# Optimization experiments

Hardware: AMD Instinct MI355X
Metric: run time of the kernel (lower is better)

## Reference

```python
import jax, jax.numpy as jnp
import numpy as np

BSZ, T, D_IN, P, H, D_OUT = 8, 4096, 512, 256, 256, 512


def setup_inputs() -> dict:
    key = jax.random.key(0)
    ks = jax.random.split(key, 8)
    x_seq = jax.random.normal(ks[0], (BSZ, T, D_IN), dtype=jnp.float32)
    # stable diagonal transition: |a| < 1 so the 4096-step recurrence does not blow up
    a = jax.random.uniform(ks[1], (H,), minval=-0.99, maxval=0.99, dtype=jnp.float32)
    B = jax.random.normal(ks[2], (P, H), dtype=jnp.float32) * 0.05
    C = jax.random.normal(ks[3], (H, P), dtype=jnp.float32) * 0.05
    Wi = jax.random.normal(ks[4], (P, D_IN), dtype=jnp.float32) * 0.05
    bi = jax.random.normal(ks[5], (P,), dtype=jnp.float32) * 0.05
    Wo = jax.random.normal(ks[6], (D_OUT, P), dtype=jnp.float32) * 0.05
    bo = jax.random.normal(ks[7], (D_OUT,), dtype=jnp.float32) * 0.05
    return {"x_seq": x_seq, "a": a, "B": B, "C": C, "Wi": Wi, "bi": bi, "Wo": Wo, "bo": bo}


def reference(x_seq, a, B, C, Wi, bi, Wo, bo):
    # proj_in + relu (eqx.nn.Linear: y = W @ x + b), vmapped over batch and time
    x_proj = jax.nn.relu(jnp.einsum("btd,pd->btp", x_seq, Wi) + bi)  # [Bsz,T,P]
    # precompute driving input u_t = B^T x_t for every step
    u = jnp.einsum("btp,ph->bth", x_proj, B)  # [Bsz,T,H]
    u_t = jnp.swapaxes(u, 0, 1)  # [T,Bsz,H] (scan over time)

    def step(h, u_step):  # h: [Bsz,H]
        h = a * h + u_step
        return h, h

    h0 = jnp.zeros((x_seq.shape[0], a.shape[0]), dtype=x_seq.dtype)
    _, hs = jax.lax.scan(step, h0, u_t)  # hs: [T,Bsz,H]
    # y_t = C^T h_t, then proj_out
    y_seq = jnp.einsum("tbh,hp->btp", hs, C)  # [Bsz,T,P]
    y_out = jnp.einsum("btp,op->bto", y_seq, Wo) + bo  # [Bsz,T,D_out]
    return y_out
```

## Files before the change

### kernel.cpp

```cpp
#include <hip/hip_runtime.h>

#define BSZN 8
#define TT 4096
#define DIN 512
#define PP 256
#define HHH 256
#define DOUT 512
#define LCH 64
#define NCH (TT / LCH)
#define NBLK (BSZN * NCH)
#define XTS 520
#define XPS 264

typedef __attribute__((ext_vector_type(8))) short bf16x8;
typedef __attribute__((ext_vector_type(4))) float f32x4;

static __device__ __forceinline__ unsigned short f2bf(float x) {
  union { float f; unsigned u; } t{x};
  unsigned r = t.u + 0x7fffu + ((t.u >> 16) & 1u);
  return (unsigned short)(r >> 16);
}


__global__ __launch_bounds__(256) void prep_k(
    const float* __restrict__ Wi, const float* __restrict__ Wo,
    const float* __restrict__ Cm, const float* __restrict__ Bm,
    unsigned short* __restrict__ Wi_t, unsigned short* __restrict__ B_t,
    unsigned short* __restrict__ C_t, unsigned short* __restrict__ Wo_t) {
  const int b = blockIdx.x, tid = threadIdx.x;
  if (b < 128) {
    const int idx = b * 1024 + tid * 4;
    const int row = idx >> 9, d = idx & 511;
    const float4 v = *(const float4*)(Wi + idx);
    uint2 w;
    w.x = (unsigned)f2bf(v.x) | ((unsigned)f2bf(v.y) << 16);
    w.y = (unsigned)f2bf(v.z) | ((unsigned)f2bf(v.w) << 16);
    const int tile = d >> 5, kc = (d >> 3) & 3, s = (kc + (row >> 1)) & 3;
    *(uint2*)(Wi_t + tile * 8192 + row * 32 + s * 8 + (d & 7)) = w;
  } else if (b < 192) {
    const int f = (b - 128) * 256 + tid;
    const int p = f >> 6, h = (f & 63) * 4;
    const float4 v = *(const float4*)(Bm + (size_t)p * HHH + h);
    const float vv[4] = {v.x, v.y, v.z, v.w};
    const int tile = p >> 5, kc = (p >> 3) & 3;
#pragma unroll
    for (int j = 0; j < 4; ++j) {
      const int row = h + j, s = (kc + (row >> 1)) & 3;
      B_t[tile * 8192 + row * 32 + s * 8 + (p & 7)] = f2bf(vv[j]);
    }
  } else if (b < 256) {
    const int f = (b - 192) * 256 + tid;
    const int h = f >> 6, p = (f & 63) * 4;
    const float4 v = *(const float4*)(Cm + (size_t)h * PP + p);
    const float vv[4] = {v.x, v.y, v.z, v.w};
    const int tile = h >> 5, kc = (h >> 3) & 3;
#pragma unroll
    for (int j = 0; j < 4; ++j) {
      const int row = p + j, s = (kc + (row >> 1)) & 3;
      C_t[tile * 8192 + row * 32 + s * 8 + (h & 7)] = f2bf(vv[j]);
    }
  } else {
    const int idx = (b - 256) * 1024 + tid * 4;
    const int o = idx >> 8, p = idx & 255;
    const float4 v = *(const float4*)(Wo + idx);
    uint2 w;
    w.x = (unsigned)f2bf(v.x) | ((unsigned)f2bf(v.y) << 16);
    w.y = (unsigned)f2bf(v.z) | ((unsigned)f2bf(v.w) << 16);
    const int tile = p >> 5, kc = (p >> 3) & 3, s = (kc + (o >> 1)) & 3;
    *(uint2*)(Wo_t + tile * 16384 + o * 32 + s * 8 + (p & 7)) = w;
  }
}

__global__ __launch_bounds__(256, 2) void s4_scan(
    const float* __restrict__ x, const float* __restrict__ a,
    const unsigned short* __restrict__ Wi_t, const float* __restrict__ bi,
    const unsigned short* __restrict__ B_t, float* __restrict__ hs0_g,
    float* __restrict__ carry_g) {
  __shared__ alignas(16) char smem[66560];
  unsigned short* xs = (unsigned short*)smem;
  unsigned short* xp = (unsigned short*)smem;

  const int tid = threadIdx.x, wave = tid >> 6, lane = tid & 63;
  const int l15 = lane & 15, q = lane >> 4;
  const int bc = blockIdx.x;
  const size_t row0 = (size_t)bc * LCH;
  const int wc = wave * 64;

  int wrot[4];
#pragma unroll
  for (int ni = 0; ni < 4; ++ni) {
    const int r = wc + ni * 16 + l15;
    wrot[ni] = r * 64 + (((q + (r >> 1)) & 3) << 4);
  }
  int xsb[4];
#pragma unroll
  for (int mi = 0; mi < 4; ++mi) xsb[mi] = (mi * 16 + l15) * (XTS * 2) + q * 16;
  int xpb[4];
#pragma unroll
  for (int mi = 0; mi < 4; ++mi) xpb[mi] = (mi * 16 + l15) * XPS + q * 8;

#pragma unroll
  for (int rr = 0; rr < 2; ++rr) {
    float4 xv[16];
#pragma unroll
    for (int i = 0; i < 16; ++i) {
      const int f = rr * 4096 + i * 256 + tid;
      xv[i] = *(const float4*)(x + (row0 + (f >> 7)) * DIN + (f & 127) * 4);
    }
#pragma unroll
    for (int i = 0; i < 16; ++i) {
      const int f = rr * 4096 + i * 256 + tid;
      uint2 w;
      w.x = (unsigned)f2bf(xv[i].x) | ((unsigned)f2bf(xv[i].y) << 16);
      w.y = (unsigned)f2bf(xv[i].z) | ((unsigned)f2bf(xv[i].w) << 16);
      *(uint2*)(xs + (f >> 7) * XTS + (f & 127) * 4) = w;
    }
  }
  __syncthreads();

  f32x4 acc[4][4];
#pragma unroll
  for (int i = 0; i < 4; ++i)
#pragma unroll
    for (int j = 0; j < 4; ++j) acc[i][j] = f32x4{0.f, 0.f, 0.f, 0.f};
  {
    const char* WiB = (const char*)Wi_t;
    for (int t = 0; t < 8; ++t) {
      bf16x8 af[4][2], bfv[4][2];
#pragma unroll
      for (int mi = 0; mi < 4; ++mi) {
        af[mi][0] = *(const bf16x8*)((const char*)xs + xsb[mi] + t * 128);
        af[mi][1] = *(const bf16x8*)((const char*)xs + xsb[mi] + t * 128 + 64);
      }
#pragma unroll
      for (int ni = 0; ni < 4; ++ni) {
        bfv[ni][0] = *(const bf16x8*)(WiB + t * 32768 + wrot[ni]);
        bfv[ni][1] = *(const bf16x8*)(WiB + t * 32768 + 16384 + wrot[ni]);
      }
#pragma unroll
      for (int kk = 0; kk < 2; ++kk)
#pragma unroll
        for (int mi = 0; mi < 4; ++mi)
#pragma unroll
          for (int ni = 0; ni < 4; ++ni)
            acc[mi][ni] = __builtin_amdgcn_mfma_f32_16x16x32_bf16(
                af[mi][kk], bfv[ni][kk], acc[mi][ni], 0, 0, 0);
    }
  }
  __syncthreads();

#pragma unroll
  for (int ni = 0; ni < 4; ++ni) {
    const int col = wc + ni * 16 + l15;
    const float bb = bi[col];
#pragma unroll
    for (int mi = 0; mi < 4; ++mi)
#pragma unroll
      for (int reg = 0; reg < 4; ++reg) {
        const int row = mi * 16 + q * 4 + reg;
        xp[row * XPS + col] = f2bf(fmaxf(acc[mi][ni][reg] + bb, 0.f));
      }
  }
  __syncthreads();

#pragma unroll
  for (int i = 0; i < 4; ++i)
#pragma unroll
    for (int j = 0; j < 4; ++j) acc[i][j] = f32x4{0.f, 0.f, 0.f, 0.f};
  {
    const char* BB = (const char*)B_t;
    for (int t = 0; t < 4; ++t) {
      bf16x8 af[4][2], bfv[4][2];
#pragma unroll
      for (int mi = 0; mi < 4; ++mi) {
        af[mi][0] = *(const bf16x8*)(xp + xpb[mi] + t * 64);
        af[mi][1] = *(const bf16x8*)(xp + xpb[mi] + t * 64 + 32);
      }
#pragma unroll
      for (int ni = 0; ni < 4; ++ni) {
        bfv[ni][0] = *(const bf16x8*)(BB + t * 32768 + wrot[ni]);
        bfv[ni][1] = *(const bf16x8*)(BB + t * 32768 + 16384 + wrot[ni]);
      }
#pragma unroll
      for (int kk = 0; kk < 2; ++kk)
#pragma unroll
        for (int mi = 0; mi < 4; ++mi)
#pragma unroll
          for (int ni = 0; ni < 4; ++ni)
            acc[mi][ni] = __builtin_amdgcn_mfma_f32_16x16x32_bf16(
                af[mi][kk], bfv[ni][kk], acc[mi][ni], 0, 0, 0);
    }
  }

  float aC[4], Wz[4];
#pragma unroll
  for (int ni = 0; ni < 4; ++ni) aC[ni] = a[wc + ni * 16 + l15];
#pragma unroll
  for (int ni = 0; ni < 4; ++ni) {
    const float A = aC[ni];
    const float A2 = A * A, A4 = A2 * A2, A8 = A4 * A4, A16 = A8 * A8;
    const float A4q = ((q & 1) ? A4 : 1.f) * ((q & 2) ? A8 : 1.f);
    float W = 0.f;
#pragma unroll
    for (int mi = 0; mi < 4; ++mi) {
      f32x4 v = acc[mi][ni];
      v.y = fmaf(A, v.x, v.y);
      v.z = fmaf(A, v.y, v.z);
      v.w = fmaf(A, v.z, v.w);
      const float E = v.w;
      const float E0 = __shfl(E, l15, 64);
      const float E1 = __shfl(E, l15 + 16, 64);
      const float E2 = __shfl(E, l15 + 32, 64);
      const float E3 = __shfl(E, l15 + 48, 64);
      const float s1 = E0, s2 = fmaf(A4, s1, E1), s3 = fmaf(A4, s2, E2);
      const float s4 = fmaf(A4, s3, E3);
      const float Sq = (q == 0) ? 0.f : (q == 1) ? s1 : (q == 2) ? s2 : s3;
      const float sin_ = fmaf(A4q, W, Sq);
      v.x = fmaf(A, sin_, v.x);
      v.y = fmaf(A2, sin_, v.y);
      v.z = fmaf(A2 * A, sin_, v.z);
      v.w = fmaf(A4, sin_, v.w);
      acc[mi][ni] = v;
      W = fmaf(A16, W, s4);
    }
    Wz[ni] = W;
  }
  if (q == 0) {
#pragma unroll
    for (int ni = 0; ni < 4; ++ni)
      carry_g[(size_t)bc * HHH + wc + ni * 16 + l15] = Wz[ni];
  }
#pragma unroll
  for (int ni = 0; ni < 4; ++ni)
#pragma unroll
    for (int mi = 0; mi < 4; ++mi) {
      const size_t idx =
          ((((size_t)bc * 4 + wave) * 16 + ni * 4 + mi) * 64 + lane) * 4;
      *(f32x4*)(hs0_g + idx) = acc[mi][ni];
    }
}

__global__ __launch_bounds__(256) void s4_prefix(
    const float* __restrict__ a, const float* __restrict__ carry_g,
    float* __restrict__ P_g) {
  const int b = blockIdx.x, t = threadIdx.x;
  float A = a[t];
#pragma unroll
  for (int j = 0; j < 6; ++j) A *= A;
  const float* cg = carry_g + (size_t)b * NCH * HHH + t;
  float* pg = P_g + (size_t)b * NCH * HHH + t;
  float cv[NCH];
#pragma unroll
  for (int c = 0; c < NCH; ++c) cv[c] = cg[(size_t)c * HHH];
  float P = 0.f;
#pragma unroll
  for (int c = 0; c < NCH; ++c) {
    pg[(size_t)c * HHH] = P;
    P = fmaf(A, P, cv[c]);
  }
}

__global__ __launch_bounds__(256, 2) void s4_out(
    const float* __restrict__ a, const float* __restrict__ hs0_g,
    const float* __restrict__ P_g, const unsigned short* __restrict__ C_t,
    const unsigned short* __restrict__ Wo_t, const float* __restrict__ bo,
    float* __restrict__ out) {
  __shared__ alignas(16) char smem[33792];
  unsigned short* hsL = (unsigned short*)smem;

  const int tid = threadIdx.x, wave = tid >> 6, lane = tid & 63;
  const int l15 = lane & 15, q = lane >> 4;
  const int bc = blockIdx.x;
  const size_t row0 = (size_t)bc * LCH;
  const int wc = wave * 64;

  int wrot[4];
#pragma unroll
  for (int ni = 0; ni < 4; ++ni) {
    const int r = wc + ni * 16 + l15;
    wrot[ni] = r * 64 + (((q + (r >> 1)) & 3) << 4);
  }
  int crot[2][4];
#pragma unroll
  for (int g = 0; g < 2; ++g)
#pragma unroll
    for (int ni = 0; ni < 4; ++ni) {
      const int r = wave * 128 + g * 64 + ni * 16 + l15;
      crot[g][ni] = r * 64 + (((q + (r >> 1)) & 3) << 4);
    }
  int xpb[4];
#pragma unroll
  for (int mi = 0; mi < 4; ++mi) xpb[mi] = (mi * 16 + l15) * XPS + q * 8;

  f32x4 acc[4][4];
#pragma unroll
  for (int ni = 0; ni < 4; ++ni)
#pragma unroll
    for (int mi = 0; mi < 4; ++mi) {
      const size_t idx =
          ((((size_t)bc * 4 + wave) * 16 + ni * 4 + mi) * 64 + lane) * 4;
      acc[mi][ni] = *(const f32x4*)(hs0_g + idx);
    }
#pragma unroll
  for (int ni = 0; ni < 4; ++ni) {
    const int col = wc + ni * 16 + l15;
    const float A = a[col];
    const float P = P_g[(size_t)bc * HHH + col];
    const float A2 = A * A, A4 = A2 * A2, A8 = A4 * A4, A16 = A8 * A8;
    const float A4q = ((q & 1) ? A4 : 1.f) * ((q & 2) ? A8 : 1.f);
    float fm = A4q * A * P;
#pragma unroll
    for (int mi = 0; mi < 4; ++mi) {
      f32x4 v = acc[mi][ni];
      v.x += fm;
      v.y = fmaf(A, fm, v.y);
      v.z = fmaf(A2, fm, v.z);
      v.w = fmaf(A2 * A, fm, v.w);
      acc[mi][ni] = v;
      fm *= A16;
    }
  }
#pragma unroll
  for (int ni = 0; ni < 4; ++ni) {
    const int col = wc + ni * 16 + l15;
#pragma unroll
    for (int mi = 0; mi < 4; ++mi)
#pragma unroll
      for (int reg = 0; reg < 4; ++reg)
        hsL[(mi * 16 + q * 4 + reg) * XPS + col] = f2bf(acc[mi][ni][reg]);
  }
  __syncthreads();

#pragma unroll
  for (int i = 0; i < 4; ++i)
#pragma unroll
    for (int j = 0; j < 4; ++j) acc[i][j] = f32x4{0.f, 0.f, 0.f, 0.f};
  {
    const char* CB = (const char*)C_t;
    for (int t = 0; t < 4; ++t) {
      bf16x8 af[4][2], bfv[4][2];
#pragma unroll
      for (int mi = 0; mi < 4; ++mi) {
        af[mi][0] = *(const bf16x8*)(hsL + xpb[mi] + t * 64);
        af[mi][1] = *(const bf16x8*)(hsL + xpb[mi] + t * 64 + 32);
      }
#pragma unroll
      for (int ni = 0; ni < 4; ++ni) {
        bfv[ni][0] = *(const bf16x8*)(CB + t * 32768 + wrot[ni]);
        bfv[ni][1] = *(const bf16x8*)(CB + t * 32768 + 16384 + wrot[ni]);
      }
#pragma unroll
      for (int kk = 0; kk < 2; ++kk)
#pragma unroll
        for (int mi = 0; mi < 4; ++mi)
#pragma unroll
          for (int ni = 0; ni < 4; ++ni)
            acc[mi][ni] = __builtin_amdgcn_mfma_f32_16x16x32_bf16(
                af[mi][kk], bfv[ni][kk], acc[mi][ni], 0, 0, 0);
    }
  }
  __syncthreads();

#pragma unroll
  for (int ni = 0; ni < 4; ++ni) {
    const int col = wc + ni * 16 + l15;
#pragma unroll
    for (int mi = 0; mi < 4; ++mi)
#pragma unroll
      for (int reg = 0; reg < 4; ++reg)
        hsL[(mi * 16 + q * 4 + reg) * XPS + col] = f2bf(acc[mi][ni][reg]);
  }
  __syncthreads();

  f32x4 oacc[2][4][4];
#pragma unroll
  for (int g = 0; g < 2; ++g)
#pragma unroll
    for (int i = 0; i < 4; ++i)
#pragma unroll
      for (int j = 0; j < 4; ++j) oacc[g][i][j] = f32x4{0.f, 0.f, 0.f, 0.f};
  {
    const char* WoB = (const char*)Wo_t;
    for (int t = 0; t < 8; ++t) {
      bf16x8 af[4], bfv[2][4];
#pragma unroll
      for (int mi = 0; mi < 4; ++mi)
        af[mi] = *(const bf16x8*)(hsL + xpb[mi] + t * 32);
#pragma unroll
      for (int g = 0; g < 2; ++g)
#pragma unroll
        for (int ni = 0; ni < 4; ++ni)
          bfv[g][ni] = *(const bf16x8*)(WoB + t * 32768 + crot[g][ni]);
#pragma unroll
      for (int g = 0; g < 2; ++g)
#pragma unroll
        for (int mi = 0; mi < 4; ++mi)
#pragma unroll
          for (int ni = 0; ni < 4; ++ni)
            oacc[g][mi][ni] = __builtin_amdgcn_mfma_f32_16x16x32_bf16(
                af[mi], bfv[g][ni], oacc[g][mi][ni], 0, 0, 0);
    }
  }
#pragma unroll
  for (int g = 0; g < 2; ++g)
#pragma unroll
    for (int ni = 0; ni < 4; ++ni) {
      const int ocol = wave * 128 + g * 64 + ni * 16 + l15;
      const float bb = bo[ocol];
#pragma unroll
      for (int mi = 0; mi < 4; ++mi)
#pragma unroll
        for (int reg = 0; reg < 4; ++reg) {
          const int row = mi * 16 + q * 4 + reg;
          out[(row0 + row) * DOUT + ocol] = oacc[g][mi][ni][reg] + bb;
        }
    }
}

extern "C" void kernel_launch(void* const* d_in, const int* in_sizes, int n_in,
                              void* d_out, int out_size, void* d_ws,
                              size_t ws_size, hipStream_t stream) {
  const float* x  = (const float*)d_in[0];
  const float* a  = (const float*)d_in[1];
  const float* Bm = (const float*)d_in[2];
  const float* Cm = (const float*)d_in[3];
  const float* Wi = (const float*)d_in[4];
  const float* bi = (const float*)d_in[5];
  const float* Wo = (const float*)d_in[6];
  const float* bo = (const float*)d_in[7];
  float* out = (float*)d_out;

  char* ws = (char*)d_ws;
  unsigned short* Wi_t = (unsigned short*)ws; ws += (size_t)PP * DIN * 2;
  unsigned short* B_t  = (unsigned short*)ws; ws += (size_t)HHH * PP * 2;
  unsigned short* C_t  = (unsigned short*)ws; ws += (size_t)HHH * PP * 2;
  unsigned short* Wo_t = (unsigned short*)ws; ws += (size_t)DOUT * PP * 2;
  float* carry_g = (float*)ws; ws += (size_t)NBLK * HHH * 4;
  float* P_g     = (float*)ws; ws += (size_t)NBLK * HHH * 4;
  float* hs0_g   = (float*)ws;

  prep_k<<<384, 256, 0, stream>>>(Wi, Wo, Cm, Bm, Wi_t, B_t, C_t, Wo_t);
  s4_scan<<<NBLK, 256, 0, stream>>>(x, a, Wi_t, bi, B_t, hs0_g, carry_g);
  s4_prefix<<<BSZN, 256, 0, stream>>>(a, carry_g, P_g);
  s4_out<<<NBLK, 256, 0, stream>>>(a, hs0_g, P_g, C_t, Wo_t, bo, out);
}
```

Baseline: 161.4 us.

## Halve scan chunk length, split x staging by K, store intermediate states in bf16

```diff
diff --git a/kernel.cpp b/kernel.cpp
--- a/kernel.cpp
+++ b/kernel.cpp
@@ -6,10 +6,9 @@
 #define PP 256
 #define HHH 256
 #define DOUT 512
-#define LCH 64
+#define LCH 32
 #define NCH (TT / LCH)
 #define NBLK (BSZN * NCH)
-#define XTS 520
 #define XPS 264
 
 typedef __attribute__((ext_vector_type(8))) short bf16x8;
@@ -71,12 +70,12 @@
   }
 }
 
-__global__ __launch_bounds__(256, 2) void s4_scan(
+__global__ __launch_bounds__(256, 4) void s4_scan(
     const float* __restrict__ x, const float* __restrict__ a,
     const unsigned short* __restrict__ Wi_t, const float* __restrict__ bi,
-    const unsigned short* __restrict__ B_t, float* __restrict__ hs0_g,
+    const unsigned short* __restrict__ B_t, unsigned int* __restrict__ hs0_g,
     float* __restrict__ carry_g) {
-  __shared__ alignas(16) char smem[66560];
+  __shared__ alignas(16) char smem[16896];
   unsigned short* xs = (unsigned short*)smem;
   unsigned short* xp = (unsigned short*)smem;
 
@@ -92,69 +91,66 @@
     const int r = wc + ni * 16 + l15;
     wrot[ni] = r * 64 + (((q + (r >> 1)) & 3) << 4);
   }
-  int xsb[4];
-#pragma unroll
-  for (int mi = 0; mi < 4; ++mi) xsb[mi] = (mi * 16 + l15) * (XTS * 2) + q * 16;
-  int xpb[4];
-#pragma unroll
-  for (int mi = 0; mi < 4; ++mi) xpb[mi] = (mi * 16 + l15) * XPS + q * 8;
-
-#pragma unroll
-  for (int rr = 0; rr < 2; ++rr) {
-    float4 xv[16];
-#pragma unroll
-    for (int i = 0; i < 16; ++i) {
-      const int f = rr * 4096 + i * 256 + tid;
-      xv[i] = *(const float4*)(x + (row0 + (f >> 7)) * DIN + (f & 127) * 4);
-    }
-#pragma unroll
-    for (int i = 0; i < 16; ++i) {
-      const int f = rr * 4096 + i * 256 + tid;
-      uint2 w;
-      w.x = (unsigned)f2bf(xv[i].x) | ((unsigned)f2bf(xv[i].y) << 16);
-      w.y = (unsigned)f2bf(xv[i].z) | ((unsigned)f2bf(xv[i].w) << 16);
-      *(uint2*)(xs + (f >> 7) * XTS + (f & 127) * 4) = w;
-    }
-  }
-  __syncthreads();
-
-  f32x4 acc[4][4];
-#pragma unroll
-  for (int i = 0; i < 4; ++i)
+  int xpb[2];
+#pragma unroll
+  for (int mi = 0; mi < 2; ++mi) xpb[mi] = (mi * 16 + l15) * XPS + q * 8;
+
+  f32x4 acc[2][4];
+#pragma unroll
+  for (int i = 0; i < 2; ++i)
 #pragma unroll
     for (int j = 0; j < 4; ++j) acc[i][j] = f32x4{0.f, 0.f, 0.f, 0.f};
-  {
-    const char* WiB = (const char*)Wi_t;
-    for (int t = 0; t < 8; ++t) {
-      bf16x8 af[4][2], bfv[4][2];
-#pragma unroll
-      for (int mi = 0; mi < 4; ++mi) {
-        af[mi][0] = *(const bf16x8*)((const char*)xs + xsb[mi] + t * 128);
-        af[mi][1] = *(const bf16x8*)((const char*)xs + xsb[mi] + t * 128 + 64);
+
+  for (int hh = 0; hh < 2; ++hh) {
+    {
+      float4 xv[8];
+#pragma unroll
+      for (int i = 0; i < 8; ++i) {
+        const int f = i * 256 + tid;
+        xv[i] = *(const float4*)(x + (row0 + (f >> 6)) * DIN + hh * 256 +
+                                 (f & 63) * 4);
+      }
+#pragma unroll
+      for (int i = 0; i < 8; ++i) {
+        const int f = i * 256 + tid;
+        uint2 w;
+        w.x = (unsigned)f2bf(xv[i].x) | ((unsigned)f2bf(xv[i].y) << 16);
+        w.y = (unsigned)f2bf(xv[i].z) | ((unsigned)f2bf(xv[i].w) << 16);
+        *(uint2*)(xs + (f >> 6) * XPS + (f & 63) * 4) = w;
+      }
+    }
+    __syncthreads();
+    const char* WiB = (const char*)Wi_t + hh * 8 * 16384;
+    for (int t = 0; t < 4; ++t) {
+      bf16x8 af[2][2], bfv[4][2];
+#pragma unroll
+      for (int mi = 0; mi < 2; ++mi) {
+        af[mi][0] = *(const bf16x8*)(xs + xpb[mi] + t * 64);
+        af[mi][1] = *(const bf16x8*)(xs + xpb[mi] + t * 64 + 32);
       }
 #pragma unroll
       for (int ni = 0; ni < 4; ++ni) {
-        bfv[ni][0] = *(const bf16x8*)(WiB + t * 32768 + wrot[ni]);
-        bfv[ni][1] = *(const bf16x8*)(WiB + t * 32768 + 16384 + wrot[ni]);
+        bfv[ni][0] = *(const bf16x8*)(WiB + (t * 2) * 16384 + wrot[ni]);
+        bfv[ni][1] = *(const bf16x8*)(WiB + (t * 2 + 1) * 16384 + wrot[ni]);
       }
 #pragma unroll
       for (int kk = 0; kk < 2; ++kk)
 #pragma unroll
-        for (int mi = 0; mi < 4; ++mi)
+        for (int mi = 0; mi < 2; ++mi)
 #pragma unroll
           for (int ni = 0; ni < 4; ++ni)
             acc[mi][ni] = __builtin_amdgcn_mfma_f32_16x16x32_bf16(
                 af[mi][kk], bfv[ni][kk], acc[mi][ni], 0, 0, 0);
     }
-  }
-  __syncthreads();
+    __syncthreads();
+  }
 
 #pragma unroll
   for (int ni = 0; ni < 4; ++ni) {
     const int col = wc + ni * 16 + l15;
     const float bb = bi[col];
 #pragma unroll
-    for (int mi = 0; mi < 4; ++mi)
+    for (int mi = 0; mi < 2; ++mi)
 #pragma unroll
       for (int reg = 0; reg < 4; ++reg) {
         const int row = mi * 16 + q * 4 + reg;
@@ -164,27 +160,27 @@
   __syncthreads();
 
 #pragma unroll
-  for (int i = 0; i < 4; ++i)
+  for (int i = 0; i < 2; ++i)
 #pragma unroll
     for (int j = 0; j < 4; ++j) acc[i][j] = f32x4{0.f, 0.f, 0.f, 0.f};
   {
     const char* BB = (const char*)B_t;
     for (int t = 0; t < 4; ++t) {
-      bf16x8 af[4][2], bfv[4][2];
-#pragma unroll
-      for (int mi = 0; mi < 4; ++mi) {
+      bf16x8 af[2][2], bfv[4][2];
+#pragma unroll
+      for (int mi = 0; mi < 2; ++mi) {
         af[mi][0] = *(const bf16x8*)(xp + xpb[mi] + t * 64);
         af[mi][1] = *(const bf16x8*)(xp + xpb[mi] + t * 64 + 32);
       }
 #pragma unroll
       for (int ni = 0; ni < 4; ++ni) {
-        bfv[ni][0] = *(const bf16x8*)(BB + t * 32768 + wrot[ni]);
-        bfv[ni][1] = *(const bf16x8*)(BB + t * 32768 + 16384 + wrot[ni]);
+        bfv[ni][0] = *(const bf16x8*)(BB + (t * 2) * 16384 + wrot[ni]);
+        bfv[ni][1] = *(const bf16x8*)(BB + (t * 2 + 1) * 16384 + wrot[ni]);
       }
 #pragma unroll
       for (int kk = 0; kk < 2; ++kk)
 #pragma unroll
-        for (int mi = 0; mi < 4; ++mi)
+        for (int mi = 0; mi < 2; ++mi)
 #pragma unroll
           for (int ni = 0; ni < 4; ++ni)
             acc[mi][ni] = __builtin_amdgcn_mfma_f32_16x16x32_bf16(
@@ -202,7 +198,7 @@
     const float A4q = ((q & 1) ? A4 : 1.f) * ((q & 2) ? A8 : 1.f);
     float W = 0.f;
 #pragma unroll
-    for (int mi = 0; mi < 4; ++mi) {
+    for (int mi = 0; mi < 2; ++mi) {
       f32x4 v = acc[mi][ni];
       v.y = fmaf(A, v.x, v.y);
       v.z = fmaf(A, v.y, v.z);
@@ -233,10 +229,14 @@
 #pragma unroll
   for (int ni = 0; ni < 4; ++ni)
 #pragma unroll
-    for (int mi = 0; mi < 4; ++mi) {
-      const size_t idx =
-          ((((size_t)bc * 4 + wave) * 16 + ni * 4 + mi) * 64 + lane) * 4;
-      *(f32x4*)(hs0_g + idx) = acc[mi][ni];
+    for (int mi = 0; mi < 2; ++mi) {
+      const f32x4 v = acc[mi][ni];
+      uint2 pk;
+      pk.x = (unsigned)f2bf(v.x) | ((unsigned)f2bf(v.y) << 16);
+      pk.y = (unsigned)f2bf(v.z) | ((unsigned)f2bf(v.w) << 16);
+      const size_t e =
+          (((size_t)bc * 4 + wave) * 8 + ni * 2 + mi) * 64 + lane;
+      *(uint2*)(hs0_g + e * 2) = pk;
     }
 }
 
@@ -246,26 +246,28 @@
   const int b = blockIdx.x, t = threadIdx.x;
   float A = a[t];
 #pragma unroll
-  for (int j = 0; j < 6; ++j) A *= A;
+  for (int j = 0; j < 5; ++j) A *= A;
   const float* cg = carry_g + (size_t)b * NCH * HHH + t;
   float* pg = P_g + (size_t)b * NCH * HHH + t;
-  float cv[NCH];
-#pragma unroll
-  for (int c = 0; c < NCH; ++c) cv[c] = cg[(size_t)c * HHH];
   float P = 0.f;
-#pragma unroll
-  for (int c = 0; c < NCH; ++c) {
-    pg[(size_t)c * HHH] = P;
-    P = fmaf(A, P, cv[c]);
-  }
-}
-
-__global__ __launch_bounds__(256, 2) void s4_out(
-    const float* __restrict__ a, const float* __restrict__ hs0_g,
+  for (int c0 = 0; c0 < NCH; c0 += 16) {
+    float cv[16];
+#pragma unroll
+    for (int i = 0; i < 16; ++i) cv[i] = cg[(size_t)(c0 + i) * HHH];
+#pragma unroll
+    for (int i = 0; i < 16; ++i) {
+      pg[(size_t)(c0 + i) * HHH] = P;
+      P = fmaf(A, P, cv[i]);
+    }
+  }
+}
+
+__global__ __launch_bounds__(256, 4) void s4_out(
+    const float* __restrict__ a, const unsigned int* __restrict__ hs0_g,
     const float* __restrict__ P_g, const unsigned short* __restrict__ C_t,
     const unsigned short* __restrict__ Wo_t, const float* __restrict__ bo,
     float* __restrict__ out) {
-  __shared__ alignas(16) char smem[33792];
+  __shared__ alignas(16) char smem[16896];
   unsigned short* hsL = (unsigned short*)smem;
 
   const int tid = threadIdx.x, wave = tid >> 6, lane = tid & 63;
@@ -288,18 +290,24 @@
       const int r = wave * 128 + g * 64 + ni * 16 + l15;
       crot[g][ni] = r * 64 + (((q + (r >> 1)) & 3) << 4);
     }
-  int xpb[4];
-#pragma unroll
-  for (int mi = 0; mi < 4; ++mi) xpb[mi] = (mi * 16 + l15) * XPS + q * 8;
-
-  f32x4 acc[4][4];
+  int xpb[2];
+#pragma unroll
+  for (int mi = 0; mi < 2; ++mi) xpb[mi] = (mi * 16 + l15) * XPS + q * 8;
+
+  f32x4 acc[2][4];
 #pragma unroll
   for (int ni = 0; ni < 4; ++ni)
 #pragma unroll
-    for (int mi = 0; mi < 4; ++mi) {
-      const size_t idx =
-          ((((size_t)bc * 4 + wave) * 16 + ni * 4 + mi) * 64 + lane) * 4;
-      acc[mi][ni] = *(const f32x4*)(hs0_g + idx);
+    for (int mi = 0; mi < 2; ++mi) {
+      const size_t e =
+          (((size_t)bc * 4 + wave) * 8 + ni * 2 + mi) * 64 + lane;
+      const uint2 pk = *(const uint2*)(hs0_g + e * 2);
+      f32x4 v;
+      v.x = __uint_as_float(pk.x << 16);
+      v.y = __uint_as_float(pk.x & 0xffff0000u);
+      v.z = __uint_as_float(pk.y << 16);
+      v.w = __uint_as_float(pk.y & 0xffff0000u);
+      acc[mi][ni] = v;
     }
 #pragma unroll
   for (int ni = 0; ni < 4; ++ni) {
@@ -310,7 +318,7 @@
     const float A4q = ((q & 1) ? A4 : 1.f) * ((q & 2) ? A8 : 1.f);
     float fm = A4q * A * P;
 #pragma unroll
-    for (int mi = 0; mi < 4; ++mi) {
+    for (int mi = 0; mi < 2; ++mi) {
       f32x4 v = acc[mi][ni];
       v.x += fm;
       v.y = fmaf(A, fm, v.y);
@@ -324,7 +332,7 @@
   for (int ni = 0; ni < 4; ++ni) {
     const int col = wc + ni * 16 + l15;
 #pragma unroll
-    for (int mi = 0; mi < 4; ++mi)
+    for (int mi = 0; mi < 2; ++mi)
 #pragma unroll
       for (int reg = 0; reg < 4; ++reg)
         hsL[(mi * 16 + q * 4 + reg) * XPS + col] = f2bf(acc[mi][ni][reg]);
@@ -332,27 +340,27 @@
   __syncthreads();
 
 #pragma unroll
-  for (int i = 0; i < 4; ++i)
+  for (int i = 0; i < 2; ++i)
 #pragma unroll
     for (int j = 0; j < 4; ++j) acc[i][j] = f32x4{0.f, 0.f, 0.f, 0.f};
   {
     const char* CB = (const char*)C_t;
     for (int t = 0; t < 4; ++t) {
-      bf16x8 af[4][2], bfv[4][2];
-#pragma unroll
-      for (int mi = 0; mi < 4; ++mi) {
+      bf16x8 af[2][2], bfv[4][2];
+#pragma unroll
+      for (int mi = 0; mi < 2; ++mi) {
         af[mi][0] = *(const bf16x8*)(hsL + xpb[mi] + t * 64);
         af[mi][1] = *(const bf16x8*)(hsL + xpb[mi] + t * 64 + 32);
       }
 #pragma unroll
       for (int ni = 0; ni < 4; ++ni) {
-        bfv[ni][0] = *(const bf16x8*)(CB + t * 32768 + wrot[ni]);
-        bfv[ni][1] = *(const bf16x8*)(CB + t * 32768 + 16384 + wrot[ni]);
+        bfv[ni][0] = *(const bf16x8*)(CB + (t * 2) * 16384 + wrot[ni]);
+        bfv[ni][1] = *(const bf16x8*)(CB + (t * 2 + 1) * 16384 + wrot[ni]);
       }
 #pragma unroll
       for (int kk = 0; kk < 2; ++kk)
 #pragma unroll
-        for (int mi = 0; mi < 4; ++mi)
+        for (int mi = 0; mi < 2; ++mi)
 #pragma unroll
           for (int ni = 0; ni < 4; ++ni)
             acc[mi][ni] = __builtin_amdgcn_mfma_f32_16x16x32_bf16(
@@ -365,56 +373,49 @@
   for (int ni = 0; ni < 4; ++ni) {
     const int col = wc + ni * 16 + l15;
 #pragma unroll
-    for (int mi = 0; mi < 4; ++mi)
+    for (int mi = 0; mi < 2; ++mi)
 #pragma unroll
       for (int reg = 0; reg < 4; ++reg)
         hsL[(mi * 16 + q * 4 + reg) * XPS + col] = f2bf(acc[mi][ni][reg]);
   }
   __syncthreads();
 
-  f32x4 oacc[2][4][4];
-#pragma unroll
-  for (int g = 0; g < 2; ++g)
-#pragma unroll
-    for (int i = 0; i < 4; ++i)
-#pragma unroll
-      for (int j = 0; j < 4; ++j) oacc[g][i][j] = f32x4{0.f, 0.f, 0.f, 0.f};
-  {
-    const char* WoB = (const char*)Wo_t;
+  const char* WoB = (const char*)Wo_t;
+#pragma unroll
+  for (int g = 0; g < 2; ++g) {
+    f32x4 oacc[2][4];
+#pragma unroll
+    for (int i = 0; i < 2; ++i)
+#pragma unroll
+      for (int j = 0; j < 4; ++j) oacc[i][j] = f32x4{0.f, 0.f, 0.f, 0.f};
     for (int t = 0; t < 8; ++t) {
-      bf16x8 af[4], bfv[2][4];
-#pragma unroll
-      for (int mi = 0; mi < 4; ++mi)
+      bf16x8 af[2], bfv[4];
+#pragma unroll
+      for (int mi = 0; mi < 2; ++mi)
         af[mi] = *(const bf16x8*)(hsL + xpb[mi] + t * 32);
 #pragma unroll
-      for (int g = 0; g < 2; ++g)
+      for (int ni = 0; ni < 4; ++ni)
+        bfv[ni] = *(const bf16x8*)(WoB + t * 32768 + crot[g][ni]);
+#pragma unroll
+      for (int mi = 0; mi < 2; ++mi)
 #pragma unroll
         for (int ni = 0; ni < 4; ++ni)
-          bfv[g][ni] = *(const bf16x8*)(WoB + t * 32768 + crot[g][ni]);
-#pragma unroll
-      for (int g = 0; g < 2; ++g)
-#pragma unroll
-        for (int mi = 0; mi < 4; ++mi)
-#pragma unroll
-          for (int ni = 0; ni < 4; ++ni)
-            oacc[g][mi][ni] = __builtin_amdgcn_mfma_f32_16x16x32_bf16(
-                af[mi], bfv[g][ni], oacc[g][mi][ni], 0, 0, 0);
-    }
-  }
-#pragma unroll
-  for (int g = 0; g < 2; ++g)
+          oacc[mi][ni] = __builtin_amdgcn_mfma_f32_16x16x32_bf16(
+              af[mi], bfv[ni], oacc[mi][ni], 0, 0, 0);
+    }
 #pragma unroll
     for (int ni = 0; ni < 4; ++ni) {
       const int ocol = wave * 128 + g * 64 + ni * 16 + l15;
       const float bb = bo[ocol];
 #pragma unroll
-      for (int mi = 0; mi < 4; ++mi)
+      for (int mi = 0; mi < 2; ++mi)
 #pragma unroll
         for (int reg = 0; reg < 4; ++reg) {
           const int row = mi * 16 + q * 4 + reg;
-          out[(row0 + row) * DOUT + ocol] = oacc[g][mi][ni][reg] + bb;
+          out[(row0 + row) * DOUT + ocol] = oacc[mi][ni][reg] + bb;
         }
     }
+  }
 }
 
 extern "C" void kernel_launch(void* const* d_in, const int* in_sizes, int n_in,
@@ -437,7 +438,7 @@
   unsigned short* Wo_t = (unsigned short*)ws; ws += (size_t)DOUT * PP * 2;
   float* carry_g = (float*)ws; ws += (size_t)NBLK * HHH * 4;
   float* P_g     = (float*)ws; ws += (size_t)NBLK * HHH * 4;
-  float* hs0_g   = (float*)ws;
+  unsigned int* hs0_g = (unsigned int*)ws;
 
   prep_k<<<384, 256, 0, stream>>>(Wi, Wo, Cm, Bm, Wi_t, B_t, C_t, Wo_t);
   s4_scan<<<NBLK, 256, 0, stream>>>(x, a, Wi_t, bi, B_t, hs0_g, carry_g);
```

New measurement: 164.2 us. No clear change (+1.7%).
